# Kernel optimization log

Hardware: AMD Instinct MI355X
Metric: run time of the kernel (lower is better)

The kernel has to match this reference:

```python
import jax, jax.numpy as jnp
import numpy as np

RADIUS = 2
P = 8 * RADIUS  # n_points = 16
PAD = RADIUS + 1

# Circular sample offsets, matching skimage local_binary_pattern:
#   rp = -R*sin(2*pi*i/P), cp = R*cos(2*pi*i/P), rounded to 8 decimals.
_ang = 2.0 * np.pi * np.arange(P) / P
_RP = np.round(-RADIUS * np.sin(_ang), 8)
_CP = np.round(RADIUS * np.cos(_ang), 8)


def lbp_var(img):
    """LBP 'var' transform: per-pixel population variance of the P
    bilinearly-interpolated circular neighbors (zero padding outside).
    img: [B, C, H, W] -> [B, C, H, W]
    """
    B, C, H, W = img.shape
    padded = jnp.pad(img, ((0, 0), (0, 0), (PAD, PAD), (PAD, PAD)))

    def shifted(dr, dc):
        # static-offset slice of the padded image == image sampled at (r+dr, c+dc)
        return padded[:, :, PAD + dr:PAD + dr + H, PAD + dc:PAD + dc + W]

    s1 = jnp.zeros_like(img)
    s2 = jnp.zeros_like(img)
    for i in range(P):  # small fixed loop over the 16 circle points
        rp, cp = float(_RP[i]), float(_CP[i])
        fr, fc = int(np.floor(rp)), int(np.floor(cp))
        tr, tc = rp - fr, cp - fc
        v = jnp.zeros_like(img)
        for (dr, dc, w) in ((fr, fc, (1 - tr) * (1 - tc)),
                            (fr, fc + 1, (1 - tr) * tc),
                            (fr + 1, fc, tr * (1 - tc)),
                            (fr + 1, fc + 1, tr * tc)):
            if w > 1e-12:  # skip exactly-zero bilinear weights (static)
                v = v + jnp.float32(w) * shifted(dr, dc)
        s1 = s1 + v
        s2 = s2 + v * v
    mean = s1 / P
    var = s2 / P - mean * mean
    return jnp.nan_to_num(var)


def reference(output, target):
    out_lbp = lbp_var(output)
    trg_lbp = lbp_var(target)
    return jnp.mean((out_lbp - trg_lbp) ** 2)


def setup_inputs() -> dict:
    key = jax.random.key(0)
    k1, k2 = jax.random.split(key)
    shape = (16, 3, 512, 512)
    return {
        "output": jax.random.uniform(k1, shape, dtype=jnp.float32),
        "target": jax.random.uniform(k2, shape, dtype=jnp.float32),
    }
```

## Files before the change

kernel.cpp:

```cpp
#include <hip/hip_runtime.h>


typedef float f2 __attribute__((ext_vector_type(2)));

#define IMG_H 512
#define IMG_W 512
#define TILE_X 64
#define TILE_Y 16
#define LDS_H  20
#define LDS_CP 72
#define LDS_SP 74

constexpr double RPV[16] = {
   0.0,        -0.76536686, -1.41421356, -1.84775907,
  -2.0,        -1.84775907, -1.41421356, -0.76536686,
   0.0,         0.76536686,  1.41421356,  1.84775907,
   2.0,         1.84775907,  1.41421356,  0.76536686
};
constexpr double CPV[16] = {
   2.0,         1.84775907,  1.41421356,  0.76536686,
   0.0,        -0.76536686, -1.41421356, -1.84775907,
  -2.0,        -1.84775907, -1.41421356, -0.76536686,
   0.0,         0.76536686,  1.41421356,  1.84775907
};

constexpr int cfloor(double x) {
  int i = (int)x;
  return (x < (double)i) ? i - 1 : i;
}

__device__ __forceinline__ f2 splat(float x) { f2 r; r.x = x; r.y = x; return r; }

template<int I>
__device__ __forceinline__ void lbp_point(const f2 (&w)[5][8], int px,
                                          f2& s1, f2& s2) {
  constexpr double rp = RPV[I], cp = CPV[I];
  constexpr int fr = cfloor(rp), fc = cfloor(cp);
  constexpr double tr = rp - (double)fr, tc = cp - (double)fc;
  constexpr double W00 = (1.0 - tr) * (1.0 - tc);
  constexpr double W01 = (1.0 - tr) * tc;
  constexpr double W10 = tr * (1.0 - tc);
  constexpr double W11 = tr * tc;
  f2 v = splat(0.0f);
  if constexpr (W00 > 1e-12)
    v = __builtin_elementwise_fma(splat((float)W00), w[fr + 2][px + fc + 2], v);
  if constexpr (W01 > 1e-12)
    v = __builtin_elementwise_fma(splat((float)W01), w[fr + 2][px + fc + 3], v);
  if constexpr (W10 > 1e-12)
    v = __builtin_elementwise_fma(splat((float)W10), w[fr + 3][px + fc + 2], v);
  if constexpr (W11 > 1e-12)
    v = __builtin_elementwise_fma(splat((float)W11), w[fr + 3][px + fc + 3], v);
  s1 = s1 + v;
  s2 = __builtin_elementwise_fma(v, v, s2);
}

__device__ __forceinline__ void lbp_all16(const f2 (&w)[5][8], int px,
                                          f2& s1, f2& s2) {
  lbp_point<0>(w, px, s1, s2);  lbp_point<1>(w, px, s1, s2);
  lbp_point<2>(w, px, s1, s2);  lbp_point<3>(w, px, s1, s2);
  lbp_point<4>(w, px, s1, s2);  lbp_point<5>(w, px, s1, s2);
  lbp_point<6>(w, px, s1, s2);  lbp_point<7>(w, px, s1, s2);
  lbp_point<8>(w, px, s1, s2);  lbp_point<9>(w, px, s1, s2);
  lbp_point<10>(w, px, s1, s2); lbp_point<11>(w, px, s1, s2);
  lbp_point<12>(w, px, s1, s2); lbp_point<13>(w, px, s1, s2);
  lbp_point<14>(w, px, s1, s2); lbp_point<15>(w, px, s1, s2);
}

__global__ __launch_bounds__(256)
void lbp_loss_kernel(const float* __restrict__ A, const float* __restrict__ B,
                     double* __restrict__ part) {
  __shared__ __align__(16) f2 tile[LDS_H][LDS_SP];
  __shared__ double bsum[4];

  const int tid = threadIdx.x;
  const int bx = blockIdx.x, by = blockIdx.y, z = blockIdx.z;
  const int row0 = by * TILE_Y - 2;
  const int col0 = bx * TILE_X - 4;
  const size_t ibase = (size_t)z * (IMG_H * IMG_W);

  const int QUADS = LDS_CP / 4;
  const int SLOTS = LDS_H * QUADS;
  for (int idx = tid; idx < SLOTS; idx += 256) {
    const int r = idx / QUADS;
    const int q = idx - r * QUADS;
    const int gr = row0 + r;
    const int gc = col0 + q * 4;
    float4 a = make_float4(0.f, 0.f, 0.f, 0.f);
    float4 b = make_float4(0.f, 0.f, 0.f, 0.f);
    if ((unsigned)gr < (unsigned)IMG_H && (unsigned)gc < (unsigned)IMG_W) {
      const size_t off = ibase + (size_t)gr * IMG_W + gc;
      a = *(const float4*)&A[off];
      b = *(const float4*)&B[off];
    }
    f2* dst = &tile[r][q * 4];
    dst[0] = f2{a.x, b.x};
    dst[1] = f2{a.y, b.y};
    dst[2] = f2{a.z, b.z};
    dst[3] = f2{a.w, b.w};
  }
  __syncthreads();

  const int tx = tid & 15;
  const int ty = tid >> 4;

  f2 w[5][8];
  #pragma unroll
  for (int r = 0; r < 5; ++r) {
    const f2* lp = &tile[ty + r][tx * 4 + 2];
    float4 q0 = *(const float4*)(lp + 0);
    float4 q1 = *(const float4*)(lp + 2);
    float4 q2 = *(const float4*)(lp + 4);
    float4 q3 = *(const float4*)(lp + 6);
    w[r][0] = f2{q0.x, q0.y}; w[r][1] = f2{q0.z, q0.w};
    w[r][2] = f2{q1.x, q1.y}; w[r][3] = f2{q1.z, q1.w};
    w[r][4] = f2{q2.x, q2.y}; w[r][5] = f2{q2.z, q2.w};
    w[r][6] = f2{q3.x, q3.y}; w[r][7] = f2{q3.z, q3.w};
  }

  float local = 0.0f;
  #pragma unroll
  for (int px = 0; px < 4; ++px) {
    f2 s1 = splat(0.0f), s2 = splat(0.0f);
    lbp_all16(w, px, s1, s2);
    f2 mean = s1 * 0.0625f;
    f2 var  = __builtin_elementwise_fma(-mean, mean, s2 * 0.0625f);
    const float d = var.x - var.y;
    local = fmaf(d, d, local);
  }

  #pragma unroll
  for (int off = 32; off > 0; off >>= 1)
    local += __shfl_down(local, off, 64);
  if ((tid & 63) == 0) bsum[tid >> 6] = (double)local;
  __syncthreads();
  if (tid == 0) {
    const int bflat = bx + gridDim.x * (by + gridDim.y * z);
    part[bflat] = bsum[0] + bsum[1] + bsum[2] + bsum[3];
  }
}

__global__ __launch_bounds__(1024)
void reduce_kernel(const double* __restrict__ part, int n,
                   float* __restrict__ out, double inv_n) {
  __shared__ double sm[16];
  double s = 0.0;
  for (int i = threadIdx.x; i < n; i += 1024) s += part[i];
  #pragma unroll
  for (int off = 32; off > 0; off >>= 1)
    s += __shfl_down(s, off, 64);
  if ((threadIdx.x & 63) == 0) sm[threadIdx.x >> 6] = s;
  __syncthreads();
  if (threadIdx.x < 16) {
    double t = sm[threadIdx.x];
    #pragma unroll
    for (int off = 8; off > 0; off >>= 1)
      t += __shfl_down(t, off, 64);
    if (threadIdx.x == 0) out[0] = (float)(t * inv_n);
  }
}

extern "C" void kernel_launch(void* const* d_in, const int* in_sizes, int n_in,
                              void* d_out, int out_size, void* d_ws, size_t ws_size,
                              hipStream_t stream) {
  const float* A = (const float*)d_in[0];
  const float* B = (const float*)d_in[1];
  float* out = (float*)d_out;
  double* part = (double*)d_ws;

  const int total = in_sizes[0];
  const int BC = total / (IMG_H * IMG_W);
  dim3 grid(IMG_W / TILE_X, IMG_H / TILE_Y, BC);
  lbp_loss_kernel<<<grid, 256, 0, stream>>>(A, B, part);

  const int nblocks = grid.x * grid.y * grid.z;
  reduce_kernel<<<1, 1024, 0, stream>>>(part, nblocks, out, 1.0 / (double)total);
}
```

Baseline: 143.3 us.

## Fuse final reduction into main kernel via last-block atomic counter

```diff
diff --git a/kernel.cpp b/kernel.cpp
--- a/kernel.cpp
+++ b/kernel.cpp
@@ -66,11 +66,13 @@
   lbp_point<14>(w, px, s1, s2); lbp_point<15>(w, px, s1, s2);
 }
 
-__global__ __launch_bounds__(256)
+__global__ __launch_bounds__(256, 4)
 void lbp_loss_kernel(const float* __restrict__ A, const float* __restrict__ B,
-                     double* __restrict__ part) {
+                     double* __restrict__ part, unsigned int* __restrict__ counter,
+                     float* __restrict__ out, int nblocks, double inv_n) {
   __shared__ __align__(16) f2 tile[LDS_H][LDS_SP];
   __shared__ double bsum[4];
+  __shared__ int lastFlag;
 
   const int tid = threadIdx.x;
   const int bx = blockIdx.x, by = blockIdx.y, z = blockIdx.z;
@@ -107,14 +109,10 @@
   #pragma unroll
   for (int r = 0; r < 5; ++r) {
     const f2* lp = &tile[ty + r][tx * 4 + 2];
-    float4 q0 = *(const float4*)(lp + 0);
-    float4 q1 = *(const float4*)(lp + 2);
-    float4 q2 = *(const float4*)(lp + 4);
-    float4 q3 = *(const float4*)(lp + 6);
-    w[r][0] = f2{q0.x, q0.y}; w[r][1] = f2{q0.z, q0.w};
-    w[r][2] = f2{q1.x, q1.y}; w[r][3] = f2{q1.z, q1.w};
-    w[r][4] = f2{q2.x, q2.y}; w[r][5] = f2{q2.z, q2.w};
-    w[r][6] = f2{q3.x, q3.y}; w[r][7] = f2{q3.z, q3.w};
+    *(float4*)&w[r][0] = *(const float4*)(lp + 0);
+    *(float4*)&w[r][2] = *(const float4*)(lp + 2);
+    *(float4*)&w[r][4] = *(const float4*)(lp + 4);
+    *(float4*)&w[r][6] = *(const float4*)(lp + 6);
   }
 
   float local = 0.0f;
@@ -133,29 +131,30 @@
     local += __shfl_down(local, off, 64);
   if ((tid & 63) == 0) bsum[tid >> 6] = (double)local;
   __syncthreads();
+
   if (tid == 0) {
     const int bflat = bx + gridDim.x * (by + gridDim.y * z);
-    part[bflat] = bsum[0] + bsum[1] + bsum[2] + bsum[3];
+    const double psum = bsum[0] + bsum[1] + bsum[2] + bsum[3];
+    __hip_atomic_store(&part[bflat], psum, __ATOMIC_RELEASE,
+                       __HIP_MEMORY_SCOPE_AGENT);
+    unsigned int old = __hip_atomic_fetch_add(counter, 1u, __ATOMIC_ACQ_REL,
+                                              __HIP_MEMORY_SCOPE_AGENT);
+    lastFlag = (old == (unsigned)(nblocks - 1));
   }
-}
+  __syncthreads();
 
-__global__ __launch_bounds__(1024)
-void reduce_kernel(const double* __restrict__ part, int n,
-                   float* __restrict__ out, double inv_n) {
-  __shared__ double sm[16];
-  double s = 0.0;
-  for (int i = threadIdx.x; i < n; i += 1024) s += part[i];
-  #pragma unroll
-  for (int off = 32; off > 0; off >>= 1)
-    s += __shfl_down(s, off, 64);
-  if ((threadIdx.x & 63) == 0) sm[threadIdx.x >> 6] = s;
-  __syncthreads();
-  if (threadIdx.x < 16) {
-    double t = sm[threadIdx.x];
+  if (lastFlag) {
+    double s = 0.0;
+    for (int i = tid; i < nblocks; i += 256)
+      s += __hip_atomic_load(&part[i], __ATOMIC_RELAXED, __HIP_MEMORY_SCOPE_AGENT);
     #pragma unroll
-    for (int off = 8; off > 0; off >>= 1)
-      t += __shfl_down(t, off, 64);
-    if (threadIdx.x == 0) out[0] = (float)(t * inv_n);
+    for (int off = 32; off > 0; off >>= 1)
+      s += __shfl_down(s, off, 64);
+    __syncthreads();
+    if ((tid & 63) == 0) bsum[tid >> 6] = s;
+    __syncthreads();
+    if (tid == 0)
+      out[0] = (float)((bsum[0] + bsum[1] + bsum[2] + bsum[3]) * inv_n);
   }
 }
 
@@ -165,13 +164,15 @@
   const float* A = (const float*)d_in[0];
   const float* B = (const float*)d_in[1];
   float* out = (float*)d_out;
-  double* part = (double*)d_ws;
+  unsigned int* counter = (unsigned int*)d_ws;
+  double* part = (double*)((char*)d_ws + 16);
+
+  hipMemsetAsync(d_ws, 0, 16, stream);
 
   const int total = in_sizes[0];
   const int BC = total / (IMG_H * IMG_W);
   dim3 grid(IMG_W / TILE_X, IMG_H / TILE_Y, BC);
-  lbp_loss_kernel<<<grid, 256, 0, stream>>>(A, B, part);
-
   const int nblocks = grid.x * grid.y * grid.z;
-  reduce_kernel<<<1, 1024, 0, stream>>>(part, nblocks, out, 1.0 / (double)total);
+  lbp_loss_kernel<<<grid, 256, 0, stream>>>(A, B, part, counter, out, nblocks,
+                                            1.0 / (double)total);
 }
```

Result: slower. 514.1 us (+258.7%).
